# Performance work log

Hardware: AMD Instinct MI355X
Metric: run time of the kernel (lower is better)

The kernel has to match this reference:

```python
import jax, jax.numpy as jnp
import numpy as np

B, S, D = 2, 2048, 2048
H = 16
HD = D // H  # 128
THETA = 10000.0


def setup_inputs() -> dict:
    key = jax.random.key(0)
    ks = jax.random.split(key, 5)
    return {
        "hidden_states": jax.random.normal(ks[0], (B, S, D), dtype=jnp.float32),
        "Wq": jax.random.normal(ks[1], (D, D), dtype=jnp.float32) * 0.02,
        "Wk": jax.random.normal(ks[2], (D, D), dtype=jnp.float32) * 0.02,
        "Wv": jax.random.normal(ks[3], (D, D), dtype=jnp.float32) * 0.02,
        "Wo": jax.random.normal(ks[4], (D, D), dtype=jnp.float32) * 0.02,
    }


def _rotate_half(x):
    x1, x2 = x[..., : HD // 2], x[..., HD // 2:]
    return jnp.concatenate([-x2, x1], axis=-1)


def _rope_cos_sin(seq_len, dtype):
    # freqs = 1/theta^(2i/d), i in [0, d/2)
    inv_freq = 1.0 / (THETA ** (jnp.arange(0, HD, 2, dtype=jnp.float32) / HD))
    ang = jnp.arange(seq_len, dtype=jnp.float32)[:, None] * inv_freq[None, :]  # [S, HD/2]
    cos = jnp.cos(ang).astype(dtype)
    sin = jnp.sin(ang).astype(dtype)
    # torch code does cos.repeat(1,1,1,2): tile halves -> [S, HD]
    cos2 = jnp.concatenate([cos, cos], axis=-1)[None, None]  # [1,1,S,HD]
    sin2 = jnp.concatenate([sin, sin], axis=-1)[None, None]
    return cos2, sin2


def reference(hidden_states, Wq, Wk, Wv, Wo):
    b, s, d = hidden_states.shape
    scale = 1.0 / np.sqrt(HD)
    # torch Linear: y = x @ W.T
    def proj(W):
        y = jnp.einsum("bsd,ed->bse", hidden_states, W)
        return y.reshape(b, s, H, HD).transpose(0, 2, 1, 3)  # [b,h,s,hd]
    q, k, v = proj(Wq), proj(Wk), proj(Wv)

    cos, sin = _rope_cos_sin(s, q.dtype)
    q = q * cos + _rotate_half(q) * sin
    k = k * cos + _rotate_half(k) * sin

    scores = jnp.einsum("bhqd,bhkd->bhqk", q, k) * scale
    # causal mask: -inf strictly above diagonal (kv_len == seq_len here)
    causal = jnp.triu(jnp.full((s, s), -jnp.inf, dtype=scores.dtype), k=1)
    scores = scores + causal[None, None]

    attn = jax.nn.softmax(scores.astype(jnp.float32), axis=-1).astype(q.dtype)
    ctx = jnp.einsum("bhqk,bhkd->bhqd", attn, v)
    ctx = ctx.transpose(0, 2, 1, 3).reshape(b, s, d)
    return jnp.einsum("bsd,ed->bse", ctx, Wo)
```

## Files before the change

kernel.cpp:

```cpp
#include <hip/hip_runtime.h>

typedef unsigned short ushort_t;
typedef __bf16 bf16x8 __attribute__((ext_vector_type(8)));
typedef float f32x4 __attribute__((ext_vector_type(4)));

#define S_LEN 2048
#define DMODEL 2048
#define NH 16
#define HDIM 128
#define BATCH 2
#define M_ROWS (BATCH * S_LEN)

__device__ __forceinline__ ushort_t f2bf(float f) {
    union { float f; unsigned u; } v; v.f = f;
    unsigned r = (v.u + 0x7fffu + ((v.u >> 16) & 1u)) >> 16;
    return (ushort_t)r;
}
__device__ __forceinline__ float bf2f(ushort_t u) {
    union { unsigned u; float f; } v; v.u = ((unsigned)u) << 16;
    return v.f;
}

__device__ __forceinline__ void async16(const void* g, void* l) {
    __builtin_amdgcn_global_load_lds(
        (const __attribute__((address_space(1))) void*)g,
        (__attribute__((address_space(3))) void*)l, 16, 0, 0);
}

__global__ void cvt_bf16(const float* __restrict__ in, ushort_t* __restrict__ out, int n4) {
    int i = blockIdx.x * blockDim.x + threadIdx.x;
    if (i >= n4) return;
    float4 f = ((const float4*)in)[i];
    ushort4 u;
    u.x = f2bf(f.x); u.y = f2bf(f.y); u.z = f2bf(f.z); u.w = f2bf(f.w);
    ((ushort4*)out)[i] = u;
}

__global__ void rope_tables(float* __restrict__ cosT, float* __restrict__ sinT) {
    int i = blockIdx.x * blockDim.x + threadIdx.x;
    int s = i >> 6, f = i & 63;
    float inv = powf(10000.0f, -(float)(2 * f) / 128.0f);
    float ang = (float)s * inv;
    cosT[i] = cosf(ang);
    sinT[i] = sinf(ang);
}

__global__ void rope_inplace(ushort_t* __restrict__ Q, ushort_t* __restrict__ K,
                             const float* __restrict__ cosT, const float* __restrict__ sinT) {
    long i = (long)blockIdx.x * blockDim.x + threadIdx.x;
    int f = (int)(i & 63);
    long t = i >> 6;
    int s = (int)(t & (S_LEN - 1));
    int bh = (int)(t >> 11);
    long base = ((long)bh * S_LEN + s) * HDIM;
    float c = cosT[s * 64 + f], sn = sinT[s * 64 + f];
    float a0 = bf2f(Q[base + f]), a1 = bf2f(Q[base + 64 + f]);
    Q[base + f]      = f2bf(a0 * c - a1 * sn);
    Q[base + 64 + f] = f2bf(a1 * c + a0 * sn);
    float b0 = bf2f(K[base + f]), b1 = bf2f(K[base + 64 + f]);
    K[base + f]      = f2bf(b0 * c - b1 * sn);
    K[base + 64 + f] = f2bf(b1 * c + b0 * sn);
}

template <int EPI>
__global__ __launch_bounds__(512) void gemm8(
    const ushort_t* __restrict__ A, const ushort_t* __restrict__ Bm,
    void* __restrict__ C0, void* __restrict__ C1, void* __restrict__ C2,
    int NB, int K) {
    __shared__ __align__(16) ushort_t As[2][128 * 64];
    __shared__ __align__(16) ushort_t Bs[2][256 * 64];
    const int tid = threadIdx.x;
    const int lane = tid & 63;
    const int w = tid >> 6;
    const int wm = w >> 2, wn = w & 3;
    const int fr = lane & 15, g = lane >> 4;
    const int cpx = NB >> 3;
    const int xcd = blockIdx.x & 7;
    const int local = blockIdx.x >> 3;
    const int brow = (local / cpx) * 128;
    const int bcol = (xcd * cpx + local % cpx) * 256;

    int aRow[2], aK[2], bRow[4], bK[4];
#pragma unroll
    for (int q = 0; q < 2; q++) {
        int d = (q * 512 + tid) * 16;
        int row = d >> 7;
        int s = d ^ ((row & 7) << 4);
        aRow[q] = row; aK[q] = (s & 127) >> 1;
    }
#pragma unroll
    for (int q = 0; q < 4; q++) {
        int d = (q * 512 + tid) * 16;
        int row = d >> 7;
        int s = d ^ ((row & 7) << 4);
        bRow[q] = row; bK[q] = (s & 127) >> 1;
    }

    f32x4 acc[4][4];
#pragma unroll
    for (int m = 0; m < 4; m++)
#pragma unroll
        for (int n = 0; n < 4; n++) acc[m][n] = (f32x4){0.f, 0.f, 0.f, 0.f};

    auto stage = [&](int buf, int k0) {
#pragma unroll
        for (int q = 0; q < 2; q++)
            async16(&A[(long)(brow + aRow[q]) * K + k0 + aK[q]], &As[buf][(q * 512 + tid) * 8]);
#pragma unroll
        for (int q = 0; q < 4; q++)
            async16(&Bm[(long)(bcol + bRow[q]) * K + k0 + bK[q]], &Bs[buf][(q * 512 + tid) * 8]);
    };
    auto rdA = [&](int buf, int m, int ks) -> bf16x8 {
        int row = wm * 64 + m * 16 + fr;
        int cb = (ks * 64 + g * 16) ^ ((row & 7) << 4);
        return *(const bf16x8*)((const char*)&As[buf][0] + row * 128 + cb);
    };
    auto rdB = [&](int buf, int n, int ks) -> bf16x8 {
        int row = wn * 64 + n * 16 + fr;
        int cb = (ks * 64 + g * 16) ^ ((row & 7) << 4);
        return *(const bf16x8*)((const char*)&Bs[buf][0] + row * 128 + cb);
    };

    const int NT = K / 64;
    stage(0, 0);
    stage(1, 64);

    for (int kt = 0; kt < NT; ++kt) {
        const int cur = kt & 1;
        if (kt + 1 < NT) {
            asm volatile("s_waitcnt vmcnt(6)" ::: "memory");
        } else {
            asm volatile("s_waitcnt vmcnt(0)" ::: "memory");
        }
        __builtin_amdgcn_sched_barrier(0);
        __builtin_amdgcn_s_barrier();
        __builtin_amdgcn_sched_barrier(0);

        bf16x8 a0[2][2], a2[2][2], bn[4][2];
#pragma unroll
        for (int m = 0; m < 2; m++)
#pragma unroll
            for (int ks = 0; ks < 2; ks++) a0[m][ks] = rdA(cur, m, ks);
#pragma unroll
        for (int n = 0; n < 2; n++)
#pragma unroll
            for (int ks = 0; ks < 2; ks++) bn[n][ks] = rdB(cur, n, ks);
        __builtin_amdgcn_s_setprio(1);
#pragma unroll
        for (int m = 0; m < 2; m++)
#pragma unroll
            for (int n = 0; n < 2; n++)
#pragma unroll
                for (int ks = 0; ks < 2; ks++)
                    acc[m][n] = __builtin_amdgcn_mfma_f32_16x16x32_bf16(a0[m][ks], bn[n][ks], acc[m][n], 0, 0, 0);
        __builtin_amdgcn_s_setprio(0);
#pragma unroll
        for (int n = 2; n < 4; n++)
#pragma unroll
            for (int ks = 0; ks < 2; ks++) bn[n][ks] = rdB(cur, n, ks);
        __builtin_amdgcn_s_setprio(1);
#pragma unroll
        for (int m = 0; m < 2; m++)
#pragma unroll
            for (int n = 2; n < 4; n++)
#pragma unroll
                for (int ks = 0; ks < 2; ks++)
                    acc[m][n] = __builtin_amdgcn_mfma_f32_16x16x32_bf16(a0[m][ks], bn[n][ks], acc[m][n], 0, 0, 0);
        __builtin_amdgcn_s_setprio(0);
#pragma unroll
        for (int m = 0; m < 2; m++)
#pragma unroll
            for (int ks = 0; ks < 2; ks++) a2[m][ks] = rdA(cur, m + 2, ks);
        __builtin_amdgcn_s_setprio(1);
#pragma unroll
        for (int m = 0; m < 2; m++)
#pragma unroll
            for (int n = 2; n < 4; n++)
#pragma unroll
                for (int ks = 0; ks < 2; ks++)
                    acc[m + 2][n] = __builtin_amdgcn_mfma_f32_16x16x32_bf16(a2[m][ks], bn[n][ks], acc[m + 2][n], 0, 0, 0);
        __builtin_amdgcn_s_setprio(0);
        __builtin_amdgcn_s_setprio(1);
#pragma unroll
        for (int m = 0; m < 2; m++)
#pragma unroll
            for (int n = 0; n < 2; n++)
#pragma unroll
                for (int ks = 0; ks < 2; ks++)
                    acc[m + 2][n] = __builtin_amdgcn_mfma_f32_16x16x32_bf16(a2[m][ks], bn[n][ks], acc[m + 2][n], 0, 0, 0);
        __builtin_amdgcn_s_setprio(0);

        __builtin_amdgcn_s_barrier();
        __builtin_amdgcn_sched_barrier(0);
        if (kt + 2 < NT) stage(cur, (kt + 2) * 64);
    }

    const int rbase = brow + wm * 64;
    if constexpr (EPI == 0) {
        const int proj = bcol >> 11;
        const int cbase = (bcol & 2047) + wn * 64;
        if (proj < 2) {
            ushort_t* dst = (ushort_t*)(proj == 0 ? C0 : C1);
#pragma unroll
            for (int m = 0; m < 4; m++)
#pragma unroll
                for (int n = 0; n < 4; n++) {
                    int c2 = cbase + n * 16 + fr;
                    int h = c2 >> 7, hd = c2 & 127;
#pragma unroll
                    for (int r = 0; r < 4; r++) {
                        int row = rbase + m * 16 + g * 4 + r;
                        int b = row >> 11, s = row & (S_LEN - 1);
                        dst[(((long)(b * NH + h) * S_LEN) + s) * HDIM + hd] = f2bf(acc[m][n][r]);
                    }
                }
        } else {
            ushort_t* dst = (ushort_t*)C2;
#pragma unroll
            for (int m = 0; m < 4; m++) {
                int row0 = rbase + m * 16 + g * 4;
                int b = row0 >> 11, s0 = row0 & (S_LEN - 1);
#pragma unroll
                for (int n = 0; n < 4; n++) {
                    int c2 = cbase + n * 16 + fr;
                    int h = c2 >> 7, hd = c2 & 127;
                    ushort4 u;
                    u.x = f2bf(acc[m][n][0]); u.y = f2bf(acc[m][n][1]);
                    u.z = f2bf(acc[m][n][2]); u.w = f2bf(acc[m][n][3]);
                    *(ushort4*)&dst[(((long)(b * NH + h) * HDIM) + hd) * S_LEN + s0] = u;
                }
            }
        }
    } else {
        float* dst = (float*)C0;
#pragma unroll
        for (int m = 0; m < 4; m++)
#pragma unroll
            for (int n = 0; n < 4; n++) {
                int col = bcol + wn * 64 + n * 16 + fr;
#pragma unroll
                for (int r = 0; r < 4; r++) {
                    int row = rbase + m * 16 + g * 4 + r;
                    dst[(long)row * DMODEL + col] = acc[m][n][r];
                }
            }
    }
}

__global__ __launch_bounds__(256) void attn_fwd_v4(
    const ushort_t* __restrict__ Q, const ushort_t* __restrict__ K,
    const ushort_t* __restrict__ Vt, ushort_t* __restrict__ ctx) {
    __shared__ __align__(16) ushort_t Ks[2][64 * 128];
    __shared__ __align__(16) ushort_t Vs[2][128 * 64];
    __shared__ __align__(16) ushort_t Pls[4][16 * 64];

    const int tid = threadIdx.x;
    const int lane = tid & 63;
    const int w = tid >> 6;
    const int g = lane >> 4;
    const int fr = lane & 15;
    const int fk = g * 8;

    const int bid = blockIdx.x;
    const int xcd = bid & 7;
    const int t6 = bid >> 3;
    const int bh = xcd + 8 * (t6 & 3);
    const int p = t6 >> 2;
    const int qtA = p, qtB = 31 - p;
    const int b = bh >> 4, h = bh & 15;

    const ushort_t* Qb = Q + (long)bh * S_LEN * HDIM;
    const ushort_t* Kb = K + (long)bh * S_LEN * HDIM;
    const ushort_t* Vb = Vt + (long)bh * HDIM * S_LEN;

    int koff[4], voff[4], kdst[4], vdst[4];
#pragma unroll
    for (int r = 0; r < 4; r++) {
        int ci = r * 256 + tid;
        int krow = ci >> 4, kwc = ci & 15;
        koff[r] = krow * HDIM + ((kwc ^ (krow & 7)) * 8);
        kdst[r] = ci * 8;
        int vrow = ci >> 3, vwc = ci & 7;
        voff[r] = vrow * S_LEN + ((vwc ^ (vrow & 7)) * 8);
        vdst[r] = ci * 8;
    }
    auto stage = [&](int buf, int kv0) {
        const ushort_t* Kg = Kb + (long)kv0 * HDIM;
        const ushort_t* Vg = Vb + kv0;
#pragma unroll
        for (int r = 0; r < 4; r++) async16(Kg + koff[r], &Ks[buf][kdst[r]]);
#pragma unroll
        for (int r = 0; r < 4; r++) async16(Vg + voff[r], &Vs[buf][vdst[r]]);
    };

    int qrow0 = qtA * 64 + w * 16;
    bf16x8 qf[4];
    auto loadQ = [&]() {
#pragma unroll
        for (int t = 0; t < 4; t++)
            qf[t] = *(const bf16x8*)&Qb[(long)(qrow0 + fr) * HDIM + t * 32 + fk];
    };
    loadQ();

    f32x4 o[8];
#pragma unroll
    for (int i = 0; i < 8; i++) o[i] = (f32x4){0.f, 0.f, 0.f, 0.f};
    float mrun = -1e30f, lrun = 0.f;

    const float scale = 0.08838834764831845f;
    long obase = ((long)b * S_LEN) * DMODEL + (long)h * HDIM;
    auto flush = [&]() {
        float inv = 1.0f / lrun;
        long rowb = obase + (long)(qrow0 + fr) * DMODEL;
#pragma unroll
        for (int dt = 0; dt < 8; dt++) {
            ushort4 u;
            u.x = f2bf(o[dt][0] * inv); u.y = f2bf(o[dt][1] * inv);
            u.z = f2bf(o[dt][2] * inv); u.w = f2bf(o[dt][3] * inv);
            *(ushort4*)&ctx[rowb + dt * 16 + g * 4] = u;
        }
    };

    const int ntA = qtA + 1;
    const int ntot = 33;

    stage(0, 0);
    __syncthreads();

    int cur = 0;
    for (int u = 0; u < ntot; ++u) {
        if (u + 1 < ntot) {
            int kvn = (u + 1 < ntA) ? (u + 1) : (u + 1 - ntA);
            stage(cur ^ 1, kvn * 64);
        }
        const int kv0 = ((u < ntA) ? u : (u - ntA)) * 64;
        if (u == ntA) {
            flush();
            qrow0 = qtB * 64 + w * 16;
            loadQ();
#pragma unroll
            for (int i = 0; i < 8; i++) o[i] = (f32x4){0.f, 0.f, 0.f, 0.f};
            mrun = -1e30f; lrun = 0.f;
        }
        if (kv0 <= qrow0 + 15) {
            f32x4 sf[4];
#pragma unroll
            for (int c = 0; c < 4; c++) sf[c] = (f32x4){0.f, 0.f, 0.f, 0.f};
            __builtin_amdgcn_s_setprio(1);
#pragma unroll
            for (int c = 0; c < 4; c++) {
                const int krow = c * 16 + fr;
#pragma unroll
                for (int tt = 0; tt < 4; tt++) {
                    bf16x8 kb = *(const bf16x8*)&Ks[cur][krow * 128 + (((tt * 4 + g) ^ (krow & 7)) * 8)];
                    sf[c] = __builtin_amdgcn_mfma_f32_16x16x32_bf16(kb, qf[tt], sf[c], 0, 0, 0);
                }
            }
            __builtin_amdgcn_s_setprio(0);
            if (kv0 + 63 <= qrow0) {
#pragma unroll
                for (int c = 0; c < 4; c++)
#pragma unroll
                    for (int r = 0; r < 4; r++) sf[c][r] *= scale;
            } else {
                const int q = qrow0 + fr;
#pragma unroll
                for (int c = 0; c < 4; c++)
#pragma unroll
                    for (int r = 0; r < 4; r++) {
                        int kv = kv0 + c * 16 + g * 4 + r;
                        sf[c][r] = (kv <= q) ? sf[c][r] * scale : -1e30f;
                    }
            }
            {
                float vmax = -1e30f;
#pragma unroll
                for (int c = 0; c < 4; c++) {
                    float t0 = fmaxf(fmaxf(sf[c][0], sf[c][1]), fmaxf(sf[c][2], sf[c][3]));
                    vmax = fmaxf(vmax, t0);
                }
                vmax = fmaxf(vmax, __shfl_xor(vmax, 16));
                vmax = fmaxf(vmax, __shfl_xor(vmax, 32));
                if (!__all(vmax - mrun <= 8.f)) {
                    float nm = fmaxf(mrun, vmax);
                    float alpha = __expf(mrun - nm);
                    mrun = nm;
                    lrun *= alpha;
#pragma unroll
                    for (int dt = 0; dt < 8; dt++) o[dt] *= alpha;
                }
                float rs = 0.f;
#pragma unroll
                for (int c = 0; c < 4; c++)
#pragma unroll
                    for (int r = 0; r < 4; r++) {
                        float pv = __expf(sf[c][r] - mrun);
                        sf[c][r] = pv;
                        rs += pv;
                    }
                rs += __shfl_xor(rs, 16);
                rs += __shfl_xor(rs, 32);
                lrun += rs;
            }
#pragma unroll
            for (int c = 0; c < 4; c++) {
                ushort4 u;
                u.x = f2bf(sf[c][0]); u.y = f2bf(sf[c][1]);
                u.z = f2bf(sf[c][2]); u.w = f2bf(sf[c][3]);
                *(ushort4*)&Pls[w][fr * 64 + ((c * 16 + g * 4) ^ ((fr & 7) << 3))] = u;
            }
            bf16x8 pa[2];
#pragma unroll
            for (int hh = 0; hh < 2; hh++)
                pa[hh] = *(const bf16x8*)&Pls[w][fr * 64 + ((hh * 32 + g * 8) ^ ((fr & 7) << 3))];
            __builtin_amdgcn_s_setprio(1);
#pragma unroll
            for (int dt = 0; dt < 8; dt++) {
                const int vrow = dt * 16 + fr;
#pragma unroll
                for (int hh = 0; hh < 2; hh++) {
                    bf16x8 vb = *(const bf16x8*)&Vs[cur][vrow * 64 + (((hh * 4 + g) ^ (vrow & 7)) * 8)];
                    o[dt] = __builtin_amdgcn_mfma_f32_16x16x32_bf16(vb, pa[hh], o[dt], 0, 0, 0);
                }
            }
            __builtin_amdgcn_s_setprio(0);
        }
        __syncthreads();
        cur ^= 1;
    }
    flush();
}

extern "C" void kernel_launch(void* const* d_in, const int* in_sizes, int n_in,
                              void* d_out, int out_size, void* d_ws, size_t ws_size,
                              hipStream_t stream) {
    const float* hs = (const float*)d_in[0];
    const float* Wq = (const float*)d_in[1];
    const float* Wk = (const float*)d_in[2];
    const float* Wv = (const float*)d_in[3];
    const float* Wo = (const float*)d_in[4];
    float* out = (float*)d_out;

    size_t off = 0;
    char* wsb = (char*)d_ws;
    auto carve = [&](size_t bytes) { void* p = wsb + off; off += bytes; return p; };

    ushort_t* Xb   = (ushort_t*)carve((size_t)M_ROWS * DMODEL * 2);
    ushort_t* Wqb  = (ushort_t*)carve((size_t)DMODEL * DMODEL * 2);
    ushort_t* Wkb  = (ushort_t*)carve((size_t)DMODEL * DMODEL * 2);
    ushort_t* Wvb  = (ushort_t*)carve((size_t)DMODEL * DMODEL * 2);
    ushort_t* Wob  = (ushort_t*)carve((size_t)DMODEL * DMODEL * 2);
    ushort_t* Qb   = (ushort_t*)carve((size_t)BATCH * NH * S_LEN * HDIM * 2);
    ushort_t* Kb   = (ushort_t*)carve((size_t)BATCH * NH * S_LEN * HDIM * 2);
    ushort_t* Vtb  = (ushort_t*)carve((size_t)BATCH * NH * S_LEN * HDIM * 2);
    ushort_t* ctxb = (ushort_t*)carve((size_t)M_ROWS * DMODEL * 2);
    float* cosT    = (float*)carve((size_t)S_LEN * 64 * 4);
    float* sinT    = (float*)carve((size_t)S_LEN * 64 * 4);

    const int nX = M_ROWS * DMODEL;
    const int nW = DMODEL * DMODEL;

    cvt_bf16<<<(nX / 4) / 256, 256, 0, stream>>>(hs, Xb, nX / 4);
    cvt_bf16<<<(nW / 4) / 256, 256, 0, stream>>>(Wq, Wqb, nW / 4);
    cvt_bf16<<<(nW / 4) / 256, 256, 0, stream>>>(Wk, Wkb, nW / 4);
    cvt_bf16<<<(nW / 4) / 256, 256, 0, stream>>>(Wv, Wvb, nW / 4);
    cvt_bf16<<<(nW / 4) / 256, 256, 0, stream>>>(Wo, Wob, nW / 4);
    rope_tables<<<(S_LEN * 64) / 256, 256, 0, stream>>>(cosT, sinT);

    gemm8<0><<<(M_ROWS / 128) * (3 * DMODEL / 256), 512, 0, stream>>>(
        Xb, Wqb, Qb, Kb, Vtb, 3 * DMODEL / 256, DMODEL);

    rope_inplace<<<(BATCH * NH * S_LEN * 64) / 256, 256, 0, stream>>>(Qb, Kb, cosT, sinT);

    attn_fwd_v4<<<512, 256, 0, stream>>>(Qb, Kb, Vtb, ctxb);

    gemm8<2><<<(M_ROWS / 128) * (DMODEL / 256), 512, 0, stream>>>(
        ctxb, Wob, out, nullptr, nullptr, DMODEL / 256, DMODEL);
}
```

Measured before the change: 294.7 us.

## Enlarge GEMM tiles to 256-row blocks and merge weight conversions into one launch

The GEMM kernel becomes templated on the N-fragment count. Blocks now cover 256 rows, with 192 columns for the QKV projection and 256 for the output projection, and each warp holds an 8xNF accumulator tile, which raises operand reuse per LDS load. The QKV grid now holds 4096/256 * 6144/192 = 512 blocks, and the output projection holds 128. The four weight fp32-to-bf16 conversions are merged into one 2D-grid launch that relies on the bf16 weight buffers being contiguous. In exchange, register and LDS use rise, which can cut occupancy, and the output GEMM grid becomes small for the number of CUs.

```diff
diff --git a/kernel.cpp b/kernel.cpp
--- a/kernel.cpp
+++ b/kernel.cpp
@@ -34,6 +34,19 @@
     ushort4 u;
     u.x = f2bf(f.x); u.y = f2bf(f.y); u.z = f2bf(f.z); u.w = f2bf(f.w);
     ((ushort4*)out)[i] = u;
+}
+
+__global__ void cvt4_bf16(const float* __restrict__ w0, const float* __restrict__ w1,
+                          const float* __restrict__ w2, const float* __restrict__ w3,
+                          ushort_t* __restrict__ out, int n4) {
+    int i = blockIdx.x * blockDim.x + threadIdx.x;
+    if (i >= n4) return;
+    int which = blockIdx.y;
+    const float* src = which == 0 ? w0 : which == 1 ? w1 : which == 2 ? w2 : w3;
+    float4 f = ((const float4*)src)[i];
+    ushort4 u;
+    u.x = f2bf(f.x); u.y = f2bf(f.y); u.z = f2bf(f.z); u.w = f2bf(f.w);
+    ((ushort4*)(out + (size_t)which * DMODEL * DMODEL))[i] = u;
 }
 
 __global__ void rope_tables(float* __restrict__ cosT, float* __restrict__ sinT) {
@@ -62,61 +75,63 @@
     K[base + 64 + f] = f2bf(b1 * c + b0 * sn);
 }
 
-template <int EPI>
-__global__ __launch_bounds__(512) void gemm8(
+template <int EPI, int NF>
+__global__ __launch_bounds__(512) void gemm256(
     const ushort_t* __restrict__ A, const ushort_t* __restrict__ Bm,
     void* __restrict__ C0, void* __restrict__ C1, void* __restrict__ C2,
     int NB, int K) {
-    __shared__ __align__(16) ushort_t As[2][128 * 64];
-    __shared__ __align__(16) ushort_t Bs[2][256 * 64];
+    __shared__ __align__(16) ushort_t As[2][256 * 64];
+    __shared__ __align__(16) ushort_t Bs[2][NF * 64 * 64];
     const int tid = threadIdx.x;
     const int lane = tid & 63;
     const int w = tid >> 6;
     const int wm = w >> 2, wn = w & 3;
     const int fr = lane & 15, g = lane >> 4;
+    const int WN = NF * 16;
+    const int BN = NF * 64;
     const int cpx = NB >> 3;
     const int xcd = blockIdx.x & 7;
     const int local = blockIdx.x >> 3;
-    const int brow = (local / cpx) * 128;
-    const int bcol = (xcd * cpx + local % cpx) * 256;
-
-    int aRow[2], aK[2], bRow[4], bK[4];
-#pragma unroll
-    for (int q = 0; q < 2; q++) {
+    const int brow = (local / cpx) * 256;
+    const int bcol = (xcd * cpx + local % cpx) * BN;
+
+    int aRow[4], aK[4], bRow[NF], bK[NF];
+#pragma unroll
+    for (int q = 0; q < 4; q++) {
         int d = (q * 512 + tid) * 16;
         int row = d >> 7;
         int s = d ^ ((row & 7) << 4);
         aRow[q] = row; aK[q] = (s & 127) >> 1;
     }
 #pragma unroll
-    for (int q = 0; q < 4; q++) {
+    for (int q = 0; q < NF; q++) {
         int d = (q * 512 + tid) * 16;
         int row = d >> 7;
         int s = d ^ ((row & 7) << 4);
         bRow[q] = row; bK[q] = (s & 127) >> 1;
     }
 
-    f32x4 acc[4][4];
-#pragma unroll
-    for (int m = 0; m < 4; m++)
-#pragma unroll
-        for (int n = 0; n < 4; n++) acc[m][n] = (f32x4){0.f, 0.f, 0.f, 0.f};
+    f32x4 acc[8][NF];
+#pragma unroll
+    for (int m = 0; m < 8; m++)
+#pragma unroll
+        for (int n = 0; n < NF; n++) acc[m][n] = (f32x4){0.f, 0.f, 0.f, 0.f};
 
     auto stage = [&](int buf, int k0) {
 #pragma unroll
-        for (int q = 0; q < 2; q++)
+        for (int q = 0; q < 4; q++)
             async16(&A[(long)(brow + aRow[q]) * K + k0 + aK[q]], &As[buf][(q * 512 + tid) * 8]);
 #pragma unroll
-        for (int q = 0; q < 4; q++)
+        for (int q = 0; q < NF; q++)
             async16(&Bm[(long)(bcol + bRow[q]) * K + k0 + bK[q]], &Bs[buf][(q * 512 + tid) * 8]);
     };
     auto rdA = [&](int buf, int m, int ks) -> bf16x8 {
-        int row = wm * 64 + m * 16 + fr;
+        int row = wm * 128 + m * 16 + fr;
         int cb = (ks * 64 + g * 16) ^ ((row & 7) << 4);
         return *(const bf16x8*)((const char*)&As[buf][0] + row * 128 + cb);
     };
     auto rdB = [&](int buf, int n, int ks) -> bf16x8 {
-        int row = wn * 64 + n * 16 + fr;
+        int row = wn * WN + n * 16 + fr;
         int cb = (ks * 64 + g * 16) ^ ((row & 7) << 4);
         return *(const bf16x8*)((const char*)&Bs[buf][0] + row * 128 + cb);
     };
@@ -128,7 +143,8 @@
     for (int kt = 0; kt < NT; ++kt) {
         const int cur = kt & 1;
         if (kt + 1 < NT) {
-            asm volatile("s_waitcnt vmcnt(6)" ::: "memory");
+            if constexpr (NF == 3) asm volatile("s_waitcnt vmcnt(7)" ::: "memory");
+            else                   asm volatile("s_waitcnt vmcnt(8)" ::: "memory");
         } else {
             asm volatile("s_waitcnt vmcnt(0)" ::: "memory");
         }
@@ -136,58 +152,49 @@
         __builtin_amdgcn_s_barrier();
         __builtin_amdgcn_sched_barrier(0);
 
-        bf16x8 a0[2][2], a2[2][2], bn[4][2];
-#pragma unroll
-        for (int m = 0; m < 2; m++)
-#pragma unroll
-            for (int ks = 0; ks < 2; ks++) a0[m][ks] = rdA(cur, m, ks);
+        bf16x8 af[8][2], bf[NF][2];
+#pragma unroll
+        for (int m = 0; m < 4; m++)
+#pragma unroll
+            for (int ks = 0; ks < 2; ks++) af[m][ks] = rdA(cur, m, ks);
 #pragma unroll
         for (int n = 0; n < 2; n++)
 #pragma unroll
-            for (int ks = 0; ks < 2; ks++) bn[n][ks] = rdB(cur, n, ks);
+            for (int ks = 0; ks < 2; ks++) bf[n][ks] = rdB(cur, n, ks);
         __builtin_amdgcn_s_setprio(1);
 #pragma unroll
-        for (int m = 0; m < 2; m++)
+        for (int m = 0; m < 4; m++)
 #pragma unroll
             for (int n = 0; n < 2; n++)
 #pragma unroll
                 for (int ks = 0; ks < 2; ks++)
-                    acc[m][n] = __builtin_amdgcn_mfma_f32_16x16x32_bf16(a0[m][ks], bn[n][ks], acc[m][n], 0, 0, 0);
+                    acc[m][n] = __builtin_amdgcn_mfma_f32_16x16x32_bf16(af[m][ks], bf[n][ks], acc[m][n], 0, 0, 0);
         __builtin_amdgcn_s_setprio(0);
 #pragma unroll
-        for (int n = 2; n < 4; n++)
-#pragma unroll
-            for (int ks = 0; ks < 2; ks++) bn[n][ks] = rdB(cur, n, ks);
+        for (int m = 4; m < 8; m++)
+#pragma unroll
+            for (int ks = 0; ks < 2; ks++) af[m][ks] = rdA(cur, m, ks);
         __builtin_amdgcn_s_setprio(1);
 #pragma unroll
-        for (int m = 0; m < 2; m++)
-#pragma unroll
-            for (int n = 2; n < 4; n++)
+        for (int m = 4; m < 8; m++)
+#pragma unroll
+            for (int n = 0; n < 2; n++)
 #pragma unroll
                 for (int ks = 0; ks < 2; ks++)
-                    acc[m][n] = __builtin_amdgcn_mfma_f32_16x16x32_bf16(a0[m][ks], bn[n][ks], acc[m][n], 0, 0, 0);
+                    acc[m][n] = __builtin_amdgcn_mfma_f32_16x16x32_bf16(af[m][ks], bf[n][ks], acc[m][n], 0, 0, 0);
         __builtin_amdgcn_s_setprio(0);
 #pragma unroll
-        for (int m = 0; m < 2; m++)
-#pragma unroll
-            for (int ks = 0; ks < 2; ks++) a2[m][ks] = rdA(cur, m + 2, ks);
+        for (int n = 2; n < NF; n++)
+#pragma unroll
+            for (int ks = 0; ks < 2; ks++) bf[n][ks] = rdB(cur, n, ks);
         __builtin_amdgcn_s_setprio(1);
 #pragma unroll
-        for (int m = 0; m < 2; m++)
-#pragma unroll
-            for (int n = 2; n < 4; n++)
+        for (int m = 0; m < 8; m++)
+#pragma unroll
+            for (int n = 2; n < NF; n++)
 #pragma unroll
                 for (int ks = 0; ks < 2; ks++)
-                    acc[m + 2][n] = __builtin_amdgcn_mfma_f32_16x16x32_bf16(a2[m][ks], bn[n][ks], acc[m + 2][n], 0, 0, 0);
-        __builtin_amdgcn_s_setprio(0);
-        __builtin_amdgcn_s_setprio(1);
-#pragma unroll
-        for (int m = 0; m < 2; m++)
-#pragma unroll
-            for (int n = 0; n < 2; n++)
-#pragma unroll
-                for (int ks = 0; ks < 2; ks++)
-                    acc[m + 2][n] = __builtin_amdgcn_mfma_f32_16x16x32_bf16(a2[m][ks], bn[n][ks], acc[m + 2][n], 0, 0, 0);
+                    acc[m][n] = __builtin_amdgcn_mfma_f32_16x16x32_bf16(af[m][ks], bf[n][ks], acc[m][n], 0, 0, 0);
         __builtin_amdgcn_s_setprio(0);
 
         __builtin_amdgcn_s_barrier();
@@ -195,35 +202,30 @@
         if (kt + 2 < NT) stage(cur, (kt + 2) * 64);
     }
 
-    const int rbase = brow + wm * 64;
+    const int rbase = brow + wm * 128;
     if constexpr (EPI == 0) {
-        const int proj = bcol >> 11;
-        const int cbase = (bcol & 2047) + wn * 64;
-        if (proj < 2) {
-            ushort_t* dst = (ushort_t*)(proj == 0 ? C0 : C1);
-#pragma unroll
-            for (int m = 0; m < 4; m++)
-#pragma unroll
-                for (int n = 0; n < 4; n++) {
-                    int c2 = cbase + n * 16 + fr;
-                    int h = c2 >> 7, hd = c2 & 127;
+#pragma unroll
+        for (int n = 0; n < NF; n++) {
+            int c2abs = bcol + wn * WN + n * 16 + fr;
+            int proj = c2abs >> 11;
+            int c2 = c2abs & 2047;
+            int h = c2 >> 7, hd = c2 & 127;
+            if (proj < 2) {
+                ushort_t* dst = (ushort_t*)(proj == 0 ? C0 : C1);
+#pragma unroll
+                for (int m = 0; m < 8; m++)
 #pragma unroll
                     for (int r = 0; r < 4; r++) {
                         int row = rbase + m * 16 + g * 4 + r;
                         int b = row >> 11, s = row & (S_LEN - 1);
                         dst[(((long)(b * NH + h) * S_LEN) + s) * HDIM + hd] = f2bf(acc[m][n][r]);
                     }
-                }
-        } else {
-            ushort_t* dst = (ushort_t*)C2;
-#pragma unroll
-            for (int m = 0; m < 4; m++) {
-                int row0 = rbase + m * 16 + g * 4;
-                int b = row0 >> 11, s0 = row0 & (S_LEN - 1);
-#pragma unroll
-                for (int n = 0; n < 4; n++) {
-                    int c2 = cbase + n * 16 + fr;
-                    int h = c2 >> 7, hd = c2 & 127;
+            } else {
+                ushort_t* dst = (ushort_t*)C2;
+#pragma unroll
+                for (int m = 0; m < 8; m++) {
+                    int row0 = rbase + m * 16 + g * 4;
+                    int b = row0 >> 11, s0 = row0 & (S_LEN - 1);
                     ushort4 u;
                     u.x = f2bf(acc[m][n][0]); u.y = f2bf(acc[m][n][1]);
                     u.z = f2bf(acc[m][n][2]); u.w = f2bf(acc[m][n][3]);
@@ -234,10 +236,10 @@
     } else {
         float* dst = (float*)C0;
 #pragma unroll
-        for (int m = 0; m < 4; m++)
-#pragma unroll
-            for (int n = 0; n < 4; n++) {
-                int col = bcol + wn * 64 + n * 16 + fr;
+        for (int m = 0; m < 8; m++)
+#pragma unroll
+            for (int n = 0; n < NF; n++) {
+                int col = bcol + wn * WN + n * 16 + fr;
 #pragma unroll
                 for (int r = 0; r < 4; r++) {
                     int row = rbase + m * 16 + g * 4 + r;
@@ -461,19 +463,16 @@
     const int nW = DMODEL * DMODEL;
 
     cvt_bf16<<<(nX / 4) / 256, 256, 0, stream>>>(hs, Xb, nX / 4);
-    cvt_bf16<<<(nW / 4) / 256, 256, 0, stream>>>(Wq, Wqb, nW / 4);
-    cvt_bf16<<<(nW / 4) / 256, 256, 0, stream>>>(Wk, Wkb, nW / 4);
-    cvt_bf16<<<(nW / 4) / 256, 256, 0, stream>>>(Wv, Wvb, nW / 4);
-    cvt_bf16<<<(nW / 4) / 256, 256, 0, stream>>>(Wo, Wob, nW / 4);
+    cvt4_bf16<<<dim3((nW / 4) / 256, 4), 256, 0, stream>>>(Wq, Wk, Wv, Wo, Wqb, nW / 4);
     rope_tables<<<(S_LEN * 64) / 256, 256, 0, stream>>>(cosT, sinT);
 
-    gemm8<0><<<(M_ROWS / 128) * (3 * DMODEL / 256), 512, 0, stream>>>(
-        Xb, Wqb, Qb, Kb, Vtb, 3 * DMODEL / 256, DMODEL);
+    gemm256<0, 3><<<(M_ROWS / 256) * (3 * DMODEL / 192), 512, 0, stream>>>(
+        Xb, Wqb, Qb, Kb, Vtb, 3 * DMODEL / 192, DMODEL);
 
     rope_inplace<<<(BATCH * NH * S_LEN * 64) / 256, 256, 0, stream>>>(Qb, Kb, cosT, sinT);
 
     attn_fwd_v4<<<512, 256, 0, stream>>>(Qb, Kb, Vtb, ctxb);
 
-    gemm8<2><<<(M_ROWS / 128) * (DMODEL / 256), 512, 0, stream>>>(
+    gemm256<2, 4><<<(M_ROWS / 256) * (DMODEL / 256), 512, 0, stream>>>(
         ctxb, Wob, out, nullptr, nullptr, DMODEL / 256, DMODEL);
 }
```

Measured after the change: 283.9 us. 3.7% less time.
